# Optimization experiments

Measured on AMD Instinct MI355X. Metric: run time of the kernel, lower is better.

## Reference

```python
import jax, jax.numpy as jnp
import numpy as np

N = 100000
E = 640000
D = 128


def _sage_conv(x, src, dst, Wp, bp, Wl, bl, Wr):
    # project=True: project + relu source features before aggregation
    h = jax.nn.relu(x @ Wp.T + bp)            # [N, D]
    msgs = h[src]                              # [E, D] gather
    summed = jax.ops.segment_sum(msgs, dst, num_segments=N)   # [N, D]
    cnt = jax.ops.segment_sum(jnp.ones((msgs.shape[0],), x.dtype), dst, num_segments=N)
    mean = summed / jnp.maximum(cnt, 1.0)[:, None]
    # lin_l on aggregated neighbors (with bias) + lin_r on root (no bias)
    return mean @ Wl.T + bl + x @ Wr.T


def setup_inputs() -> dict:
    key = jax.random.key(0)
    ks = jax.random.split(key, 16)
    s = 1.0 / np.sqrt(D)
    x = jax.random.normal(ks[0], (N, D), dtype=jnp.float32)
    edge_index = jax.random.randint(ks[1], (2, E), 0, N, dtype=jnp.int64)
    params = {}
    for i, base in enumerate(["conv0", "conv1"]):
        params[base + "_Wp"] = jax.random.uniform(ks[2 + 5 * i], (D, D), jnp.float32, -s, s)
        params[base + "_bp"] = jax.random.uniform(ks[3 + 5 * i], (D,), jnp.float32, -s, s)
        params[base + "_Wl"] = jax.random.uniform(ks[4 + 5 * i], (D, D), jnp.float32, -s, s)
        params[base + "_bl"] = jax.random.uniform(ks[5 + 5 * i], (D,), jnp.float32, -s, s)
        params[base + "_Wr"] = jax.random.uniform(ks[6 + 5 * i], (D, D), jnp.float32, -s, s)
    return {"x": x, "edge_index": edge_index, **params}


def reference(x, edge_index,
              conv0_Wp, conv0_bp, conv0_Wl, conv0_bl, conv0_Wr,
              conv1_Wp, conv1_bp, conv1_Wl, conv1_bl, conv1_Wr):
    src, dst = edge_index[0], edge_index[1]
    h = _sage_conv(x, src, dst, conv0_Wp, conv0_bp, conv0_Wl, conv0_bl, conv0_Wr)
    h = jax.nn.relu(h)
    return _sage_conv(h, src, dst, conv1_Wp, conv1_bp, conv1_Wl, conv1_bl, conv1_Wr)
```

## Files before the change

kernel.cpp:

```cpp
#include <hip/hip_runtime.h>

#define DD 128

typedef _Float16 f16;
typedef __attribute__((ext_vector_type(8))) _Float16 v8h;
typedef __attribute__((ext_vector_type(4))) _Float16 v4h;
typedef __attribute__((ext_vector_type(4))) float f32x4;

static inline int cdiv(int a, int b) { return (a + b - 1) / b; }


__global__ __launch_bounds__(256) void zero_kernel(int* __restrict__ p, int n) {
    int i = blockIdx.x * 256 + threadIdx.x;
    if (i < n) p[i] = 0;
}


__global__ __launch_bounds__(256) void count_kernel(const int* __restrict__ dst, int E,
                                                    int* __restrict__ cnt) {
    int e = blockIdx.x * 256 + threadIdx.x;
    if (e < E) atomicAdd(&cnt[dst[e]], 1);
}

__global__ __launch_bounds__(256) void scan1(const int* __restrict__ cnt, int N,
                                             int* __restrict__ bsum) {
    __shared__ int s[256];
    int i = blockIdx.x * 256 + threadIdx.x;
    s[threadIdx.x] = (i < N) ? cnt[i] : 0;
    __syncthreads();
    for (int off = 128; off > 0; off >>= 1) {
        if (threadIdx.x < off) s[threadIdx.x] += s[threadIdx.x + off];
        __syncthreads();
    }
    if (threadIdx.x == 0) bsum[blockIdx.x] = s[0];
}

__global__ __launch_bounds__(512) void scan2(const int* __restrict__ bsum, int NB,
                                             int* __restrict__ boff) {
    __shared__ int s[512];
    int t = threadIdx.x;
    int v = (t < NB) ? bsum[t] : 0;
    s[t] = v;
    __syncthreads();
    for (int off = 1; off < 512; off <<= 1) {
        int x = (t >= off) ? s[t - off] : 0;
        __syncthreads();
        s[t] += x;
        __syncthreads();
    }
    if (t < NB) boff[t] = s[t] - v;
}

__global__ __launch_bounds__(256) void scan3(const int* __restrict__ cnt,
                                             const int* __restrict__ boff, int N,
                                             int* __restrict__ off) {
    __shared__ int s[256];
    int t = threadIdx.x;
    int i = blockIdx.x * 256 + t;
    int v = (i < N) ? cnt[i] : 0;
    s[t] = v;
    __syncthreads();
    for (int o = 1; o < 256; o <<= 1) {
        int x = (t >= o) ? s[t - o] : 0;
        __syncthreads();
        s[t] += x;
        __syncthreads();
    }
    int excl = s[t] - v + boff[blockIdx.x];
    if (i < N) off[i] = excl;
    if (i == N - 1) off[N] = excl + v;
}

__global__ __launch_bounds__(256) void fill_kernel(const int* __restrict__ src,
                                                   const int* __restrict__ dst, int E,
                                                   const int* __restrict__ off,
                                                   int* __restrict__ cnt,
                                                   int* __restrict__ csr) {
    int e = blockIdx.x * 256 + threadIdx.x;
    if (e < E) {
        int d = dst[e];
        int p = atomicSub(&cnt[d], 1) - 1;
        csr[off[d] + p] = src[e];
    }
}


__global__ __launch_bounds__(256) void cvt_w_kernel(const float* __restrict__ W0,
                                                    const float* __restrict__ W1,
                                                    const float* __restrict__ W2,
                                                    const float* __restrict__ W3,
                                                    const float* __restrict__ W4,
                                                    const float* __restrict__ W5,
                                                    f16* __restrict__ out) {
    int mat = blockIdx.x >> 4;
    const float* W = mat == 0 ? W0 : mat == 1 ? W1 : mat == 2 ? W2
                   : mat == 3 ? W3 : mat == 4 ? W4 : W5;
    int base = (blockIdx.x & 15) * 1024 + threadIdx.x * 4;
    float4 v = *(const float4*)(W + base);
    v4h o;
    o[0] = (f16)v.x; o[1] = (f16)v.y; o[2] = (f16)v.z; o[3] = (f16)v.w;
    *(v4h*)(out + mat * 16384 + base) = o;
}

__global__ __launch_bounds__(256) void cvt_x_kernel(const float* __restrict__ x,
                                                    f16* __restrict__ out, int n8) {
    int i = blockIdx.x * 256 + threadIdx.x;
    if (i >= n8) return;
    float4 a = *(const float4*)(x + (size_t)i * 8);
    float4 b = *(const float4*)(x + (size_t)i * 8 + 4);
    v8h r;
    r[0] = (f16)a.x; r[1] = (f16)a.y; r[2] = (f16)a.z; r[3] = (f16)a.w;
    r[4] = (f16)b.x; r[5] = (f16)b.y; r[6] = (f16)b.z; r[7] = (f16)b.w;
    *(v8h*)(out + (size_t)i * 8) = r;
}


__global__ __launch_bounds__(256) void aggregate_kernel(const f16* __restrict__ h,
                                                        const int* __restrict__ off,
                                                        const int* __restrict__ csr,
                                                        f16* __restrict__ mean, int N) {
    int l = threadIdx.x & 63;
    int g = l >> 4, c = l & 15;
    int stride = gridDim.x * 4;
    for (int n = blockIdx.x * 4 + (threadIdx.x >> 6); n < N; n += stride) {
        int s = off[n], e = off[n + 1];
        float acc[8] = {0.f, 0.f, 0.f, 0.f, 0.f, 0.f, 0.f, 0.f};
        for (int i = s + g; i < e; i += 4) {
            int idx = csr[i];
            v8h v = *(const v8h*)(h + (size_t)idx * DD + c * 8);
#pragma unroll
            for (int j = 0; j < 8; ++j) acc[j] += (float)v[j];
        }
#pragma unroll
        for (int j = 0; j < 8; ++j) {
            acc[j] += __shfl_xor(acc[j], 16);
            acc[j] += __shfl_xor(acc[j], 32);
        }
        int deg = e - s;
        float inv = 1.0f / (float)(deg > 0 ? deg : 1);
        if (g == 0) {
            v8h o;
#pragma unroll
            for (int j = 0; j < 8; ++j) o[j] = (f16)(acc[j] * inv);
            *(v8h*)(mean + (size_t)n * DD + c * 8) = o;
        }
    }
}


__device__ inline void stage_w(const f16* __restrict__ Wg, f16* __restrict__ smem, int t) {
#pragma unroll
    for (int i = 0; i < 8; ++i) {
        int idx16 = i * 256 + t;
        int col = idx16 >> 4, c16 = idx16 & 15;
        int sc = c16 ^ (col & 7);
        uint4 v = *(const uint4*)(Wg + idx16 * 8);
        *(uint4*)(smem + col * DD + sc * 8) = v;
    }
}

__device__ inline v8h read_b(const f16* __restrict__ smem, int ct, int ki, int l) {
    int col = ct * 16 + (l & 15);
    int c16 = ki * 4 + (l >> 4);
    int sc = c16 ^ (col & 7);
    return *(const v8h*)(smem + col * DD + sc * 8);
}

__device__ inline v8h load_frag16(const f16* __restrict__ A, int row, int kb, int M) {
    if (row >= M) {
        v8h z = {};
        return z;
    }
    return *(const v8h*)(A + (size_t)row * DD + kb);
}


__global__ __launch_bounds__(256) void proj_gemm(const f16* __restrict__ A,
                                                 const f16* __restrict__ W1,
                                                 const float* __restrict__ bias,
                                                 f16* __restrict__ OUT, int M) {
    __shared__ f16 WS[DD * DD];
    int t = threadIdx.x, l = t & 63, w = t >> 6;
    int row0 = blockIdx.x * 128 + w * 32;
    int r = l & 15, cg = l >> 4;

    stage_w(W1, WS, t);

    v8h af[2][4];
#pragma unroll
    for (int rt = 0; rt < 2; ++rt)
#pragma unroll
        for (int ki = 0; ki < 4; ++ki)
            af[rt][ki] = load_frag16(A, row0 + rt * 16 + r, ki * 32 + cg * 8, M);
    __syncthreads();

    f32x4 acc[2][8];
#pragma unroll
    for (int ct = 0; ct < 8; ++ct) {
        float bv = bias[ct * 16 + r];
        f32x4 b4 = {bv, bv, bv, bv};
        acc[0][ct] = b4;
        acc[1][ct] = b4;
    }

#pragma unroll
    for (int ct = 0; ct < 8; ++ct)
#pragma unroll
        for (int ki = 0; ki < 4; ++ki) {
            v8h b = read_b(WS, ct, ki, l);
            acc[0][ct] = __builtin_amdgcn_mfma_f32_16x16x32_f16(af[0][ki], b, acc[0][ct], 0, 0, 0);
            acc[1][ct] = __builtin_amdgcn_mfma_f32_16x16x32_f16(af[1][ki], b, acc[1][ct], 0, 0, 0);
        }

#pragma unroll
    for (int rt = 0; rt < 2; ++rt)
#pragma unroll
        for (int ct = 0; ct < 8; ++ct)
#pragma unroll
            for (int j = 0; j < 4; ++j) {
                int row = row0 + rt * 16 + cg * 4 + j;
                if (row < M)
                    OUT[(size_t)row * DD + ct * 16 + r] = (f16)fmaxf(acc[rt][ct][j], 0.f);
            }
}


template <typename TO, bool RELU>
__global__ __launch_bounds__(256) void dual_gemm(const f16* __restrict__ A,
                                                 const f16* __restrict__ Wl,
                                                 const float* __restrict__ bias,
                                                 const f16* __restrict__ B,
                                                 const f16* __restrict__ Wr,
                                                 TO* __restrict__ OUT, int M) {
    __shared__ f16 WS[DD * DD];
    int t = threadIdx.x, l = t & 63, w = t >> 6;
    int row0 = blockIdx.x * 128 + w * 32;
    int r = l & 15, cg = l >> 4;

    stage_w(Wl, WS, t);

    v8h afA[2][4], afB[2][4];
#pragma unroll
    for (int rt = 0; rt < 2; ++rt)
#pragma unroll
        for (int ki = 0; ki < 4; ++ki) {
            int row = row0 + rt * 16 + r, kb = ki * 32 + cg * 8;
            afA[rt][ki] = load_frag16(A, row, kb, M);
            afB[rt][ki] = load_frag16(B, row, kb, M);
        }
    __syncthreads();

    f32x4 acc[2][8];
#pragma unroll
    for (int ct = 0; ct < 8; ++ct) {
        float bv = bias[ct * 16 + r];
        f32x4 b4 = {bv, bv, bv, bv};
        acc[0][ct] = b4;
        acc[1][ct] = b4;
    }

#pragma unroll
    for (int ct = 0; ct < 8; ++ct)
#pragma unroll
        for (int ki = 0; ki < 4; ++ki) {
            v8h b = read_b(WS, ct, ki, l);
            acc[0][ct] = __builtin_amdgcn_mfma_f32_16x16x32_f16(afA[0][ki], b, acc[0][ct], 0, 0, 0);
            acc[1][ct] = __builtin_amdgcn_mfma_f32_16x16x32_f16(afA[1][ki], b, acc[1][ct], 0, 0, 0);
        }

    __syncthreads();
    stage_w(Wr, WS, t);
    __syncthreads();

#pragma unroll
    for (int ct = 0; ct < 8; ++ct)
#pragma unroll
        for (int ki = 0; ki < 4; ++ki) {
            v8h b = read_b(WS, ct, ki, l);
            acc[0][ct] = __builtin_amdgcn_mfma_f32_16x16x32_f16(afB[0][ki], b, acc[0][ct], 0, 0, 0);
            acc[1][ct] = __builtin_amdgcn_mfma_f32_16x16x32_f16(afB[1][ki], b, acc[1][ct], 0, 0, 0);
        }

#pragma unroll
    for (int rt = 0; rt < 2; ++rt)
#pragma unroll
        for (int ct = 0; ct < 8; ++ct)
#pragma unroll
            for (int j = 0; j < 4; ++j) {
                int row = row0 + rt * 16 + cg * 4 + j;
                if (row < M) {
                    float v = acc[rt][ct][j];
                    if (RELU) v = fmaxf(v, 0.f);
                    OUT[(size_t)row * DD + ct * 16 + r] = (TO)v;
                }
            }
}


extern "C" void kernel_launch(void* const* d_in, const int* in_sizes, int n_in,
                              void* d_out, int out_size, void* d_ws, size_t ws_size,
                              hipStream_t stream) {
    const float* x = (const float*)d_in[0];
    const int* ei = (const int*)d_in[1];
    const float* Wp0 = (const float*)d_in[2];
    const float* bp0 = (const float*)d_in[3];
    const float* Wl0 = (const float*)d_in[4];
    const float* bl0 = (const float*)d_in[5];
    const float* Wr0 = (const float*)d_in[6];
    const float* Wp1 = (const float*)d_in[7];
    const float* bp1 = (const float*)d_in[8];
    const float* Wl1 = (const float*)d_in[9];
    const float* bl1 = (const float*)d_in[10];
    const float* Wr1 = (const float*)d_in[11];

    int N = in_sizes[0] / DD;
    int E = in_sizes[1] / 2;
    const int* src = ei;
    const int* dst = ei + E;

    char* ws = (char*)d_ws;
    size_t o = 0;
    auto alloc = [&](size_t bytes) {
        size_t r = o;
        o = (o + bytes + 255) & ~(size_t)255;
        return r;
    };
    f16* w16 = (f16*)(ws + alloc((size_t)6 * DD * DD * 2));
    int* cnt = (int*)(ws + alloc((size_t)N * 4));
    int* off = (int*)(ws + alloc((size_t)(N + 1) * 4));
    int NB = cdiv(N, 256);
    int* bsum = (int*)(ws + alloc((size_t)NB * 4));
    int* boff = (int*)(ws + alloc((size_t)NB * 4));
    int* csr = (int*)(ws + alloc((size_t)E * 4));
    f16* mean = (f16*)(ws + alloc((size_t)N * DD * 2));
    f16* y1 = (f16*)(ws + alloc((size_t)N * DD * 2));
    f16* h = (f16*)d_out;
    f16* x16 = (f16*)((char*)d_out + (size_t)N * DD * 2);
    (void)ws_size;

    zero_kernel<<<NB, 256, 0, stream>>>(cnt, N);
    count_kernel<<<cdiv(E, 256), 256, 0, stream>>>(dst, E, cnt);
    scan1<<<NB, 256, 0, stream>>>(cnt, N, bsum);
    scan2<<<1, 512, 0, stream>>>(bsum, NB, boff);
    scan3<<<NB, 256, 0, stream>>>(cnt, boff, N, off);
    fill_kernel<<<cdiv(E, 256), 256, 0, stream>>>(src, dst, E, off, cnt, csr);

    cvt_w_kernel<<<96, 256, 0, stream>>>(Wp0, Wl0, Wr0, Wp1, Wl1, Wr1, w16);
    const f16* wp0 = w16 + 0 * 16384;
    const f16* wl0 = w16 + 1 * 16384;
    const f16* wr0 = w16 + 2 * 16384;
    const f16* wp1 = w16 + 3 * 16384;
    const f16* wl1 = w16 + 4 * 16384;
    const f16* wr1 = w16 + 5 * 16384;

    cvt_x_kernel<<<cdiv(N * DD / 8, 256), 256, 0, stream>>>(x, x16, N * DD / 8);

    int GB = cdiv(N, 128);
    const int AGG_GRID = 2048;
    proj_gemm<<<GB, 256, 0, stream>>>(x16, wp0, bp0, h, N);
    aggregate_kernel<<<AGG_GRID, 256, 0, stream>>>(h, off, csr, mean, N);
    dual_gemm<f16, true><<<GB, 256, 0, stream>>>(mean, wl0, bl0, x16, wr0, y1, N);
    proj_gemm<<<GB, 256, 0, stream>>>(y1, wp1, bp1, h, N);
    aggregate_kernel<<<AGG_GRID, 256, 0, stream>>>(h, off, csr, mean, N);
    dual_gemm<float, false><<<GB, 256, 0, stream>>>(mean, wl1, bl1, y1, wr1, (float*)d_out, N);
}
```

Baseline: 243.9 us.

## Fuse layer-0 output GEMM with layer-1 projection GEMM; one-node-per-wave aggregation grid

Adds a dualproj_gemm kernel that computes the layer-0 output (mean@Wl + bl + x@Wr, relu) and then, keeping the 128-row tile in shared memory, runs the layer-1 projection (relu(y@Wp + bp)). This removes a separate proj_gemm launch and its re-read of y1 from global memory. Shared memory is reused for three weight matrices, which adds extra barriers per block. The aggregate kernel also drops its grid-stride loop and launches one wave per node with a grid of N/4 blocks.

```diff
diff --git a/kernel.cpp b/kernel.cpp
--- a/kernel.cpp
+++ b/kernel.cpp
@@ -5,6 +5,7 @@
 typedef _Float16 f16;
 typedef __attribute__((ext_vector_type(8))) _Float16 v8h;
 typedef __attribute__((ext_vector_type(4))) _Float16 v4h;
+typedef __attribute__((ext_vector_type(2))) _Float16 f16x2;
 typedef __attribute__((ext_vector_type(4))) float f32x4;
 
 static inline int cdiv(int a, int b) { return (a + b - 1) / b; }
@@ -119,31 +120,30 @@
                                                         const int* __restrict__ off,
                                                         const int* __restrict__ csr,
                                                         f16* __restrict__ mean, int N) {
+    int n = blockIdx.x * 4 + (threadIdx.x >> 6);
     int l = threadIdx.x & 63;
     int g = l >> 4, c = l & 15;
-    int stride = gridDim.x * 4;
-    for (int n = blockIdx.x * 4 + (threadIdx.x >> 6); n < N; n += stride) {
-        int s = off[n], e = off[n + 1];
-        float acc[8] = {0.f, 0.f, 0.f, 0.f, 0.f, 0.f, 0.f, 0.f};
-        for (int i = s + g; i < e; i += 4) {
-            int idx = csr[i];
-            v8h v = *(const v8h*)(h + (size_t)idx * DD + c * 8);
-#pragma unroll
-            for (int j = 0; j < 8; ++j) acc[j] += (float)v[j];
-        }
-#pragma unroll
-        for (int j = 0; j < 8; ++j) {
-            acc[j] += __shfl_xor(acc[j], 16);
-            acc[j] += __shfl_xor(acc[j], 32);
-        }
-        int deg = e - s;
-        float inv = 1.0f / (float)(deg > 0 ? deg : 1);
-        if (g == 0) {
-            v8h o;
-#pragma unroll
-            for (int j = 0; j < 8; ++j) o[j] = (f16)(acc[j] * inv);
-            *(v8h*)(mean + (size_t)n * DD + c * 8) = o;
-        }
+    if (n >= N) return;
+    int s = off[n], e = off[n + 1];
+    float acc[8] = {0.f, 0.f, 0.f, 0.f, 0.f, 0.f, 0.f, 0.f};
+    for (int i = s + g; i < e; i += 4) {
+        int idx = csr[i];
+        v8h v = *(const v8h*)(h + (size_t)idx * DD + c * 8);
+#pragma unroll
+        for (int j = 0; j < 8; ++j) acc[j] += (float)v[j];
+    }
+#pragma unroll
+    for (int j = 0; j < 8; ++j) {
+        acc[j] += __shfl_xor(acc[j], 16);
+        acc[j] += __shfl_xor(acc[j], 32);
+    }
+    int deg = e - s;
+    float inv = 1.0f / (float)(deg > 0 ? deg : 1);
+    if (g == 0) {
+        v8h o;
+#pragma unroll
+        for (int j = 0; j < 8; ++j) o[j] = (f16)(acc[j] * inv);
+        *(v8h*)(mean + (size_t)n * DD + c * 8) = o;
     }
 }
 
@@ -293,6 +293,125 @@
                     if (RELU) v = fmaxf(v, 0.f);
                     OUT[(size_t)row * DD + ct * 16 + r] = (TO)v;
                 }
+            }
+}
+
+
+__global__ __launch_bounds__(256) void dualproj_gemm(const f16* __restrict__ A,
+                                                     const f16* __restrict__ Wl,
+                                                     const float* __restrict__ bl,
+                                                     const f16* __restrict__ B,
+                                                     const f16* __restrict__ Wr,
+                                                     f16* __restrict__ Y,
+                                                     const f16* __restrict__ Wp,
+                                                     const float* __restrict__ bp,
+                                                     f16* __restrict__ H, int M) {
+    __shared__ f16 WS[DD * DD];
+    int t = threadIdx.x, l = t & 63, w = t >> 6;
+    int row0 = blockIdx.x * 128 + w * 32;
+    int r = l & 15, cg = l >> 4;
+
+    stage_w(Wl, WS, t);
+
+    v8h afA[2][4], afB[2][4];
+#pragma unroll
+    for (int rt = 0; rt < 2; ++rt)
+#pragma unroll
+        for (int ki = 0; ki < 4; ++ki) {
+            int row = row0 + rt * 16 + r, kb = ki * 32 + cg * 8;
+            afA[rt][ki] = load_frag16(A, row, kb, M);
+            afB[rt][ki] = load_frag16(B, row, kb, M);
+        }
+    __syncthreads();
+
+    f32x4 acc[2][8];
+#pragma unroll
+    for (int ct = 0; ct < 8; ++ct) {
+        float bv = bl[ct * 16 + r];
+        f32x4 b4 = {bv, bv, bv, bv};
+        acc[0][ct] = b4;
+        acc[1][ct] = b4;
+    }
+
+#pragma unroll
+    for (int ct = 0; ct < 8; ++ct)
+#pragma unroll
+        for (int ki = 0; ki < 4; ++ki) {
+            v8h b = read_b(WS, ct, ki, l);
+            acc[0][ct] = __builtin_amdgcn_mfma_f32_16x16x32_f16(afA[0][ki], b, acc[0][ct], 0, 0, 0);
+            acc[1][ct] = __builtin_amdgcn_mfma_f32_16x16x32_f16(afA[1][ki], b, acc[1][ct], 0, 0, 0);
+        }
+
+    __syncthreads();
+    stage_w(Wr, WS, t);
+    __syncthreads();
+
+#pragma unroll
+    for (int ct = 0; ct < 8; ++ct)
+#pragma unroll
+        for (int ki = 0; ki < 4; ++ki) {
+            v8h b = read_b(WS, ct, ki, l);
+            acc[0][ct] = __builtin_amdgcn_mfma_f32_16x16x32_f16(afB[0][ki], b, acc[0][ct], 0, 0, 0);
+            acc[1][ct] = __builtin_amdgcn_mfma_f32_16x16x32_f16(afB[1][ki], b, acc[1][ct], 0, 0, 0);
+        }
+
+    __syncthreads();
+#pragma unroll
+    for (int rt = 0; rt < 2; ++rt)
+#pragma unroll
+        for (int ct = 0; ct < 8; ++ct)
+#pragma unroll
+            for (int j = 0; j < 4; ++j) {
+                int brow = w * 32 + rt * 16 + cg * 4 + j;
+                int col = ct * 16 + r;
+                f16 hv = (f16)fmaxf(acc[rt][ct][j], 0.f);
+                int c16 = col >> 3;
+                WS[brow * DD + (((c16 ^ (brow & 7)) << 3) | (col & 7))] = hv;
+                int grow = blockIdx.x * 128 + brow;
+                if (grow < M) Y[(size_t)grow * DD + col] = hv;
+            }
+    __syncthreads();
+
+    v8h af2[2][4];
+#pragma unroll
+    for (int rt = 0; rt < 2; ++rt)
+#pragma unroll
+        for (int ki = 0; ki < 4; ++ki) {
+            int brow = w * 32 + rt * 16 + r;
+            af2[rt][ki] = *(const v8h*)(WS + brow * DD + (((ki * 4 + cg) ^ (brow & 7)) << 3));
+        }
+    __syncthreads();
+
+    stage_w(Wp, WS, t);
+
+    f32x4 acc2[2][8];
+#pragma unroll
+    for (int ct = 0; ct < 8; ++ct) {
+        float bv = bp[ct * 16 + r];
+        f32x4 b4 = {bv, bv, bv, bv};
+        acc2[0][ct] = b4;
+        acc2[1][ct] = b4;
+    }
+    __syncthreads();
+
+#pragma unroll
+    for (int ct = 0; ct < 8; ++ct)
+#pragma unroll
+        for (int ki = 0; ki < 4; ++ki) {
+            v8h b = read_b(WS, ct, ki, l);
+            acc2[0][ct] = __builtin_amdgcn_mfma_f32_16x16x32_f16(af2[0][ki], b, acc2[0][ct], 0, 0, 0);
+            acc2[1][ct] = __builtin_amdgcn_mfma_f32_16x16x32_f16(af2[1][ki], b, acc2[1][ct], 0, 0, 0);
+        }
+
+#pragma unroll
+    for (int rt = 0; rt < 2; ++rt)
+#pragma unroll
+        for (int ct = 0; ct < 8; ++ct)
+#pragma unroll
+            for (int j = 0; j < 4; ++j) {
+                int row = row0 + rt * 16 + cg * 4 + j;
+                if (row < M)
+                    H[(size_t)row * DD + ct * 16 + r] = (f16)fmaxf(acc2[rt][ct][j], 0.f);
             }
 }
 
@@ -356,11 +475,9 @@
     cvt_x_kernel<<<cdiv(N * DD / 8, 256), 256, 0, stream>>>(x, x16, N * DD / 8);
 
     int GB = cdiv(N, 128);
-    const int AGG_GRID = 2048;
     proj_gemm<<<GB, 256, 0, stream>>>(x16, wp0, bp0, h, N);
-    aggregate_kernel<<<AGG_GRID, 256, 0, stream>>>(h, off, csr, mean, N);
-    dual_gemm<f16, true><<<GB, 256, 0, stream>>>(mean, wl0, bl0, x16, wr0, y1, N);
-    proj_gemm<<<GB, 256, 0, stream>>>(y1, wp1, bp1, h, N);
-    aggregate_kernel<<<AGG_GRID, 256, 0, stream>>>(h, off, csr, mean, N);
+    aggregate_kernel<<<cdiv(N, 4), 256, 0, stream>>>(h, off, csr, mean, N);
+    dualproj_gemm<<<GB, 256, 0, stream>>>(mean, wl0, bl0, x16, wr0, y1, wp1, bp1, h, N);
+    aggregate_kernel<<<cdiv(N, 4), 256, 0, stream>>>(h, off, csr, mean, N);
     dual_gemm<float, false><<<GB, 256, 0, stream>>>(mean, wl1, bl1, y1, wr1, (float*)d_out, N);
 }
```

New measurement: 243.0 us. About the same (-0.4%).

## Fuse prep kernels and replace three-pass scan with atomic-cursor offsets

Applied to the files above, without the earlier changes.

Merges the x conversion, weight conversion and degree counting into one launch. The three-kernel prefix scan becomes a single kernel that takes each block's base offset from an atomic cursor and stores a per-node degree array. The aggregation kernel now uses one warp per node across a full grid instead of a grid-stride loop. This removes several small launches and their serialization, at the cost of CSR segments no longer being laid out in node order, which may reduce locality when reading csr.

```diff
diff --git a/kernel.cpp b/kernel.cpp
--- a/kernel.cpp
+++ b/kernel.cpp
@@ -16,45 +16,47 @@
 }
 
 
-__global__ __launch_bounds__(256) void count_kernel(const int* __restrict__ dst, int E,
-                                                    int* __restrict__ cnt) {
-    int e = blockIdx.x * 256 + threadIdx.x;
-    if (e < E) atomicAdd(&cnt[dst[e]], 1);
-}
-
-__global__ __launch_bounds__(256) void scan1(const int* __restrict__ cnt, int N,
-                                             int* __restrict__ bsum) {
+__global__ __launch_bounds__(256) void bigprep_kernel(
+    const float* __restrict__ x, f16* __restrict__ x16, int n8,
+    const float* __restrict__ W0, const float* __restrict__ W1,
+    const float* __restrict__ W2, const float* __restrict__ W3,
+    const float* __restrict__ W4, const float* __restrict__ W5,
+    f16* __restrict__ w16,
+    const int* __restrict__ dst, int E, int* __restrict__ cnt,
+    int nbx) {
+    int b = blockIdx.x;
+    if (b < nbx) {
+        int i = b * 256 + threadIdx.x;
+        if (i >= n8) return;
+        float4 a = *(const float4*)(x + (size_t)i * 8);
+        float4 c = *(const float4*)(x + (size_t)i * 8 + 4);
+        v8h r;
+        r[0] = (f16)a.x; r[1] = (f16)a.y; r[2] = (f16)a.z; r[3] = (f16)a.w;
+        r[4] = (f16)c.x; r[5] = (f16)c.y; r[6] = (f16)c.z; r[7] = (f16)c.w;
+        *(v8h*)(x16 + (size_t)i * 8) = r;
+    } else if (b < nbx + 96) {
+        int bb = b - nbx;
+        int mat = bb >> 4;
+        const float* W = mat == 0 ? W0 : mat == 1 ? W1 : mat == 2 ? W2
+                       : mat == 3 ? W3 : mat == 4 ? W4 : W5;
+        int base = (bb & 15) * 1024 + threadIdx.x * 4;
+        float4 v = *(const float4*)(W + base);
+        v4h o;
+        o[0] = (f16)v.x; o[1] = (f16)v.y; o[2] = (f16)v.z; o[3] = (f16)v.w;
+        *(v4h*)(w16 + mat * 16384 + base) = o;
+    } else {
+        int e = (b - nbx - 96) * 256 + threadIdx.x;
+        if (e < E) atomicAdd(&cnt[dst[e]], 1);
+    }
+}
+
+
+__global__ __launch_bounds__(256) void offs_kernel(const int* __restrict__ cnt, int N,
+                                                   int* __restrict__ off,
+                                                   int* __restrict__ deg,
+                                                   int* __restrict__ cursor) {
     __shared__ int s[256];
-    int i = blockIdx.x * 256 + threadIdx.x;
-    s[threadIdx.x] = (i < N) ? cnt[i] : 0;
-    __syncthreads();
-    for (int off = 128; off > 0; off >>= 1) {
-        if (threadIdx.x < off) s[threadIdx.x] += s[threadIdx.x + off];
-        __syncthreads();
-    }
-    if (threadIdx.x == 0) bsum[blockIdx.x] = s[0];
-}
-
-__global__ __launch_bounds__(512) void scan2(const int* __restrict__ bsum, int NB,
-                                             int* __restrict__ boff) {
-    __shared__ int s[512];
-    int t = threadIdx.x;
-    int v = (t < NB) ? bsum[t] : 0;
-    s[t] = v;
-    __syncthreads();
-    for (int off = 1; off < 512; off <<= 1) {
-        int x = (t >= off) ? s[t - off] : 0;
-        __syncthreads();
-        s[t] += x;
-        __syncthreads();
-    }
-    if (t < NB) boff[t] = s[t] - v;
-}
-
-__global__ __launch_bounds__(256) void scan3(const int* __restrict__ cnt,
-                                             const int* __restrict__ boff, int N,
-                                             int* __restrict__ off) {
-    __shared__ int s[256];
+    __shared__ int base;
     int t = threadIdx.x;
     int i = blockIdx.x * 256 + t;
     int v = (i < N) ? cnt[i] : 0;
@@ -66,10 +68,14 @@
         s[t] += x;
         __syncthreads();
     }
-    int excl = s[t] - v + boff[blockIdx.x];
-    if (i < N) off[i] = excl;
-    if (i == N - 1) off[N] = excl + v;
-}
+    if (t == 255) base = atomicAdd(cursor, s[255]);
+    __syncthreads();
+    if (i < N) {
+        off[i] = base + s[t] - v;
+        deg[i] = v;
+    }
+}
+
 
 __global__ __launch_bounds__(256) void fill_kernel(const int* __restrict__ src,
                                                    const int* __restrict__ dst, int E,
@@ -85,65 +91,34 @@
 }
 
 
-__global__ __launch_bounds__(256) void cvt_w_kernel(const float* __restrict__ W0,
-                                                    const float* __restrict__ W1,
-                                                    const float* __restrict__ W2,
-                                                    const float* __restrict__ W3,
-                                                    const float* __restrict__ W4,
-                                                    const float* __restrict__ W5,
-                                                    f16* __restrict__ out) {
-    int mat = blockIdx.x >> 4;
-    const float* W = mat == 0 ? W0 : mat == 1 ? W1 : mat == 2 ? W2
-                   : mat == 3 ? W3 : mat == 4 ? W4 : W5;
-    int base = (blockIdx.x & 15) * 1024 + threadIdx.x * 4;
-    float4 v = *(const float4*)(W + base);
-    v4h o;
-    o[0] = (f16)v.x; o[1] = (f16)v.y; o[2] = (f16)v.z; o[3] = (f16)v.w;
-    *(v4h*)(out + mat * 16384 + base) = o;
-}
-
-__global__ __launch_bounds__(256) void cvt_x_kernel(const float* __restrict__ x,
-                                                    f16* __restrict__ out, int n8) {
-    int i = blockIdx.x * 256 + threadIdx.x;
-    if (i >= n8) return;
-    float4 a = *(const float4*)(x + (size_t)i * 8);
-    float4 b = *(const float4*)(x + (size_t)i * 8 + 4);
-    v8h r;
-    r[0] = (f16)a.x; r[1] = (f16)a.y; r[2] = (f16)a.z; r[3] = (f16)a.w;
-    r[4] = (f16)b.x; r[5] = (f16)b.y; r[6] = (f16)b.z; r[7] = (f16)b.w;
-    *(v8h*)(out + (size_t)i * 8) = r;
-}
-
-
 __global__ __launch_bounds__(256) void aggregate_kernel(const f16* __restrict__ h,
                                                         const int* __restrict__ off,
+                                                        const int* __restrict__ deg,
                                                         const int* __restrict__ csr,
                                                         f16* __restrict__ mean, int N) {
+    int n = blockIdx.x * 4 + (threadIdx.x >> 6);
     int l = threadIdx.x & 63;
     int g = l >> 4, c = l & 15;
-    int stride = gridDim.x * 4;
-    for (int n = blockIdx.x * 4 + (threadIdx.x >> 6); n < N; n += stride) {
-        int s = off[n], e = off[n + 1];
-        float acc[8] = {0.f, 0.f, 0.f, 0.f, 0.f, 0.f, 0.f, 0.f};
-        for (int i = s + g; i < e; i += 4) {
-            int idx = csr[i];
-            v8h v = *(const v8h*)(h + (size_t)idx * DD + c * 8);
-#pragma unroll
-            for (int j = 0; j < 8; ++j) acc[j] += (float)v[j];
-        }
-#pragma unroll
-        for (int j = 0; j < 8; ++j) {
-            acc[j] += __shfl_xor(acc[j], 16);
-            acc[j] += __shfl_xor(acc[j], 32);
-        }
-        int deg = e - s;
-        float inv = 1.0f / (float)(deg > 0 ? deg : 1);
-        if (g == 0) {
-            v8h o;
-#pragma unroll
-            for (int j = 0; j < 8; ++j) o[j] = (f16)(acc[j] * inv);
-            *(v8h*)(mean + (size_t)n * DD + c * 8) = o;
-        }
+    if (n >= N) return;
+    int s = off[n], d = deg[n], e = s + d;
+    float acc[8] = {0.f, 0.f, 0.f, 0.f, 0.f, 0.f, 0.f, 0.f};
+    for (int i = s + g; i < e; i += 4) {
+        int idx = csr[i];
+        v8h v = *(const v8h*)(h + (size_t)idx * DD + c * 8);
+#pragma unroll
+        for (int j = 0; j < 8; ++j) acc[j] += (float)v[j];
+    }
+#pragma unroll
+    for (int j = 0; j < 8; ++j) {
+        acc[j] += __shfl_xor(acc[j], 16);
+        acc[j] += __shfl_xor(acc[j], 32);
+    }
+    float inv = 1.0f / (float)(d > 0 ? d : 1);
+    if (g == 0) {
+        v8h o;
+#pragma unroll
+        for (int j = 0; j < 8; ++j) o[j] = (f16)(acc[j] * inv);
+        *(v8h*)(mean + (size_t)n * DD + c * 8) = o;
     }
 }
 
@@ -326,11 +301,9 @@
         return r;
     };
     f16* w16 = (f16*)(ws + alloc((size_t)6 * DD * DD * 2));
-    int* cnt = (int*)(ws + alloc((size_t)N * 4));
-    int* off = (int*)(ws + alloc((size_t)(N + 1) * 4));
-    int NB = cdiv(N, 256);
-    int* bsum = (int*)(ws + alloc((size_t)NB * 4));
-    int* boff = (int*)(ws + alloc((size_t)NB * 4));
+    int* cnt = (int*)(ws + alloc((size_t)(N + 1) * 4));
+    int* off = (int*)(ws + alloc((size_t)N * 4));
+    int* deg = (int*)(ws + alloc((size_t)N * 4));
     int* csr = (int*)(ws + alloc((size_t)E * 4));
     f16* mean = (f16*)(ws + alloc((size_t)N * DD * 2));
     f16* y1 = (f16*)(ws + alloc((size_t)N * DD * 2));
@@ -338,14 +311,12 @@
     f16* x16 = (f16*)((char*)d_out + (size_t)N * DD * 2);
     (void)ws_size;
 
-    zero_kernel<<<NB, 256, 0, stream>>>(cnt, N);
-    count_kernel<<<cdiv(E, 256), 256, 0, stream>>>(dst, E, cnt);
-    scan1<<<NB, 256, 0, stream>>>(cnt, N, bsum);
-    scan2<<<1, 512, 0, stream>>>(bsum, NB, boff);
-    scan3<<<NB, 256, 0, stream>>>(cnt, boff, N, off);
-    fill_kernel<<<cdiv(E, 256), 256, 0, stream>>>(src, dst, E, off, cnt, csr);
-
-    cvt_w_kernel<<<96, 256, 0, stream>>>(Wp0, Wl0, Wr0, Wp1, Wl1, Wr1, w16);
+    int NB = cdiv(N, 256);
+    int EB = cdiv(E, 256);
+    int n8 = N * DD / 8;
+    int nbx = cdiv(n8, 256);
+    int GB = cdiv(N, 128);
+
     const f16* wp0 = w16 + 0 * 16384;
     const f16* wl0 = w16 + 1 * 16384;
     const f16* wr0 = w16 + 2 * 16384;
@@ -353,14 +324,16 @@
     const f16* wl1 = w16 + 4 * 16384;
     const f16* wr1 = w16 + 5 * 16384;
 
-    cvt_x_kernel<<<cdiv(N * DD / 8, 256), 256, 0, stream>>>(x, x16, N * DD / 8);
-
-    int GB = cdiv(N, 128);
-    const int AGG_GRID = 2048;
+    zero_kernel<<<cdiv(N + 1, 256), 256, 0, stream>>>(cnt, N + 1);
+    bigprep_kernel<<<nbx + 96 + EB, 256, 0, stream>>>(
+        x, x16, n8, Wp0, Wl0, Wr0, Wp1, Wl1, Wr1, w16, dst, E, cnt, nbx);
+    offs_kernel<<<NB, 256, 0, stream>>>(cnt, N, off, deg, &cnt[N]);
+    fill_kernel<<<EB, 256, 0, stream>>>(src, dst, E, off, cnt, csr);
+
     proj_gemm<<<GB, 256, 0, stream>>>(x16, wp0, bp0, h, N);
-    aggregate_kernel<<<AGG_GRID, 256, 0, stream>>>(h, off, csr, mean, N);
+    aggregate_kernel<<<cdiv(N, 4), 256, 0, stream>>>(h, off, deg, csr, mean, N);
     dual_gemm<f16, true><<<GB, 256, 0, stream>>>(mean, wl0, bl0, x16, wr0, y1, N);
     proj_gemm<<<GB, 256, 0, stream>>>(y1, wp1, bp1, h, N);
-    aggregate_kernel<<<AGG_GRID, 256, 0, stream>>>(h, off, csr, mean, N);
+    aggregate_kernel<<<cdiv(N, 4), 256, 0, stream>>>(h, off, deg, csr, mean, N);
     dual_gemm<float, false><<<GB, 256, 0, stream>>>(mean, wl1, bl1, y1, wr1, (float*)d_out, N);
 }
```

New measurement: 247.3 us. No clear change (+1.4%).
